# Optimization experiments

Hardware: AMD Instinct MI355X
Metric: run time of the kernel (lower is better)

The kernel has to match this reference:

```python
import jax, jax.numpy as jnp
import numpy as np

N_U = 100000; N_I = 100000; D = 64; Q = 5
N_E = 2000000; L = 2; B = 4096; P = 10
TEMP = 0.2; LAM1 = 0.2; LAM2 = 0.2
DROPOUT = 0.1; EPS = 0.1


def setup_inputs() -> dict:
    key = jax.random.key(0)
    ks = jax.random.split(key, 20)
    s = 0.05  # xavier-ish init scale
    return {
        'E_u_0': jax.random.normal(ks[0], (N_U, D), jnp.float32) * s,
        'E_i_0': jax.random.normal(ks[1], (N_I, D), jnp.float32) * s,
        'adj_vals': jax.random.uniform(ks[2], (N_E,), jnp.float32) * 0.05,
        'u_mul_s': jax.random.normal(ks[3], (N_U, Q), jnp.float32) * s,
        'v_mul_s': jax.random.normal(ks[4], (N_I, Q), jnp.float32) * s,
        'ut': jax.random.normal(ks[5], (Q, N_U), jnp.float32) * s,
        'vt': jax.random.normal(ks[6], (Q, N_I), jnp.float32) * s,
        'W_nn': jax.random.normal(ks[7], (D, D), jnp.float32) * s,
        'W_dd': jax.random.normal(ks[8], (D, D), jnp.float32) * s,
        'W_ng': jax.random.normal(ks[9], (L, D, D), jnp.float32) * s,
        'W_dg': jax.random.normal(ks[10], (L, D, D), jnp.float32) * s,
        'W_nd': jax.random.normal(ks[11], (L, D, D), jnp.float32) * s,
        'adj_rows': jax.random.randint(ks[12], (N_E,), 0, N_U),
        'adj_cols': jax.random.randint(ks[13], (N_E,), 0, N_I),
        'uids': jax.random.randint(ks[14], (B,), 0, N_U),
        'iids': jax.random.randint(ks[15], (B,), 0, N_I),
        'pos': jax.random.randint(ks[16], (B, P), 0, N_I),
        'neg': jax.random.randint(ks[17], (B, P), 0, N_I),
    }


def _act(x):  # LeakyReLU(0.5)
    return jnp.where(x >= 0, x, 0.5 * x)


def _l2n(x):  # F.normalize(p=2, dim=1)
    return x / jnp.maximum(jnp.linalg.norm(x, axis=1, keepdims=True), 1e-12)


def _spmm(vals, rows, cols, X, n_out):
    # out[r] = sum_e vals[e] * X[cols[e]]
    return jax.ops.segment_sum(vals[:, None] * X[cols], rows, num_segments=n_out)


def _info_nce(gnn_raw, hyper_raw, W, mask):
    gnn = _l2n(gnn_raw)
    hyper = _l2n(hyper_raw) @ W
    pos_score = jnp.exp(jnp.sum(gnn * hyper, axis=1) / TEMP)
    neg_score = jnp.exp(gnn @ hyper.T / TEMP).sum(axis=1)
    return (-jnp.log(pos_score / (neg_score + 1e-8) + 1e-8) * mask).sum()


def _mk_mask(k):
    return (jax.random.uniform(k, (B,)) > 0.5).astype(jnp.float32)


def _forward(E_u_0, E_i_0, adj_vals, u_mul_s, v_mul_s, ut, vt, W_nn, W_dd, W_ng, W_dg, W_nd,
             adj_rows, adj_cols, uids, iids, pos, neg):
    rkey = jax.random.key(42)
    keep = 1.0 - DROPOUT
    E_u_list = [E_u_0]; E_i_list = [E_i_0]
    Z_u_list = [None]; Z_i_list = [None]
    Z_du_list = [None]; Z_di_list = [None]
    G_u_list = [None]; G_i_list = [None]
    for _ in range(L):
        rkey, k1, k2, k3, k4 = jax.random.split(rkey, 5)
        Eu_p, Ei_p = E_u_list[-1], E_i_list[-1]
        # sparse dropout (independent masks, as in torch code) + spmm + LeakyReLU
        v1 = adj_vals * jax.random.bernoulli(k1, keep, adj_vals.shape) / keep
        Z_du = _act(_spmm(v1, adj_rows, adj_cols, Ei_p, N_U))
        v2 = adj_vals * jax.random.bernoulli(k2, keep, adj_vals.shape) / keep
        Z_di = _act(_spmm(v2, adj_cols, adj_rows, Eu_p, N_I))
        # noise-augmented view
        Z_u = _act(_spmm(adj_vals, adj_rows, adj_cols, Ei_p, N_U))
        Z_u = Z_u + jnp.sign(Z_u) * _l2n(jax.random.uniform(k3, Eu_p.shape)) * EPS
        Z_i = _act(_spmm(adj_vals, adj_cols, adj_rows, Eu_p, N_I))
        Z_i = Z_i + jnp.sign(Z_i) * _l2n(jax.random.uniform(k4, Ei_p.shape)) * EPS
        # SVD (global) view
        G_u = _act(u_mul_s @ (vt @ Ei_p))
        G_i = _act(v_mul_s @ (ut @ Eu_p))
        Z_u_list.append(Z_u); Z_i_list.append(Z_i)
        Z_du_list.append(Z_du); Z_di_list.append(Z_di)
        G_u_list.append(G_u); G_i_list.append(G_i)
        E_u_list.append(Z_u + Z_du + Eu_p)
        E_i_list.append(Z_i + Z_di + Ei_p)
    E_u = E_u_list[0]
    for t in E_u_list[1:]:
        E_u = E_u + t
    E_i = E_i_list[0]
    for t in E_i_list[1:]:
        E_i = E_i + t

    mkey = jax.random.key(7)
    def L_loss(ids, Zl, Gl, Wstack, key):
        out = jnp.float32(0.0)
        for l in range(1, L + 1):
            key, km = jax.random.split(key)
            out = out + _info_nce(Zl[l][ids], Gl[l][ids], Wstack[l - 1], _mk_mask(km))
        return out, key
    def inter_loss(ids, Zl, W, key):
        key, km = jax.random.split(key)
        return _info_nce(Zl[1][ids], Zl[2][ids], W, _mk_mask(km)), key

    loss_n_u, mkey = L_loss(uids, Z_u_list, G_u_list, W_ng, mkey)
    loss_n_i, mkey = L_loss(iids, Z_i_list, G_i_list, W_ng, mkey)
    loss_nn_u, mkey = inter_loss(uids, Z_u_list, W_nn, mkey)
    loss_nn_i, mkey = inter_loss(iids, Z_i_list, W_nn, mkey)
    loss_d_u, mkey = L_loss(uids, Z_du_list, G_u_list, W_dg, mkey)
    loss_d_i, mkey = L_loss(iids, Z_di_list, G_i_list, W_dg, mkey)
    loss_dd_u, mkey = inter_loss(uids, Z_du_list, W_dd, mkey)
    loss_dd_i, mkey = inter_loss(iids, Z_di_list, W_dd, mkey)
    loss_nd_u, mkey = L_loss(uids, Z_u_list, Z_du_list, W_nd, mkey)
    loss_nd_i, mkey = L_loss(iids, Z_i_list, Z_di_list, W_nd, mkey)
    loss_n = loss_n_u + loss_n_i
    loss_d = loss_d_u + loss_d_i
    loss_nn = loss_nn_u + loss_nn_i
    loss_dd = loss_dd_u + loss_dd_i
    loss_nd = loss_nd_u + loss_nd_i

    # U_IConstLoss, vectorized over the batch
    u_emb = E_u[uids]                       # [B, D]
    pos_emb = E_i[pos]                      # [B, P, D]
    neg_emb = E_i[neg]                      # [B, P, D]
    pos_sc = jnp.einsum('bd,bpd->bp', u_emb, pos_emb)
    neg_sc = jnp.einsum('bd,bpd->bp', u_emb, neg_emb)
    pos_d = pos_sc.min(axis=1)
    neg_d = neg_sc.max(axis=1)
    hard = jnp.where(neg_d - pos_d > 0.005, 10.0 * (neg_d - pos_d), 0.0)
    bpr = jnp.maximum(1.0 - pos_sc + neg_sc, 0.0).sum(axis=1)
    loss_r = (bpr + hard).sum() / B

    loss = loss_r + LAM1 * (loss_n + loss_d) + LAM2 * (loss_nn + loss_dd + loss_nd)
    return (loss, loss_r, loss_d, loss_n)


def reference(E_u_0, E_i_0, adj_vals, u_mul_s, v_mul_s, ut, vt, W_nn, W_dd, W_ng, W_dg, W_nd,
              adj_rows, adj_cols, uids, iids, pos, neg):
    return _forward(E_u_0, E_i_0, adj_vals, u_mul_s, v_mul_s, ut, vt, W_nn, W_dd, W_ng, W_dg, W_nd,
                    adj_rows, adj_cols, uids, iids, pos, neg)
```

## Files before the change

### kernel.cpp

```cpp
#include <hip/hip_runtime.h>
#include <hip/hip_bf16.h>
#include <cstdint>

#define C_NU 100000
#define C_NI 100000
#define C_DIM 64
#define C_Q 5
#define C_NE 2000000
#define C_B 4096
#define C_P 10
#define NROW 100000
#define NCB 196
#define NCHK 256
#define CHUNK 7813

typedef unsigned short u16;
typedef unsigned char u8;
typedef __attribute__((ext_vector_type(8))) short short8;
typedef __attribute__((ext_vector_type(4))) float f32x4;

__device__ static inline int rfl(int v) { return __builtin_amdgcn_readfirstlane(v); }
__device__ static inline uint32_t rflu(uint32_t v) {
  return (uint32_t)__builtin_amdgcn_readfirstlane((int)v);
}

__host__ __device__ static inline void tf2x32(uint32_t k0, uint32_t k1,
                                              uint32_t& x0, uint32_t& x1) {
  uint32_t k2 = k0 ^ k1 ^ 0x1BD11BDAu;
#define TFR(r) { x0 += x1; x1 = (x1 << r) | (x1 >> (32 - r)); x1 ^= x0; }
  x0 += k0; x1 += k1;
  TFR(13) TFR(15) TFR(26) TFR(6)
  x0 += k1; x1 += k2 + 1u;
  TFR(17) TFR(29) TFR(16) TFR(24)
  x0 += k2; x1 += k0 + 2u;
  TFR(13) TFR(15) TFR(26) TFR(6)
  x0 += k0; x1 += k1 + 3u;
  TFR(17) TFR(29) TFR(16) TFR(24)
  x0 += k1; x1 += k2 + 4u;
  TFR(13) TFR(15) TFR(26) TFR(6)
  x0 += k2; x1 += k0 + 5u;
#undef TFR
}

__device__ static inline float tf_uniform(uint32_t k0, uint32_t k1, uint32_t idx) {
  uint32_t x0 = 0u, x1 = idx;
  tf2x32(k0, k1, x0, x1);
  uint32_t bits = x0 ^ x1;
  return __uint_as_float((bits >> 9) | 0x3F800000u) - 1.0f;
}

__device__ static inline float leaky(float x) { return x >= 0.f ? x : 0.5f * x; }

__device__ static inline u16 f2bf(float f) {
  uint32_t x = __float_as_uint(f);
  return (u16)((x + 0x7FFFu + ((x >> 16) & 1u)) >> 16);
}
__device__ static inline float bf2f(u16 u) {
  return __uint_as_float((uint32_t)u << 16);
}

__device__ static inline u8 f2fp8(float x) {
  float t = x * 256.f;
  uint32_t sgn = (__float_as_uint(t) >> 24) & 0x80u;
  float a = fabsf(t) * 0x1p-120f;
  uint32_t u = __float_as_uint(a);
  u += 0x7FFFFu + ((u >> 20) & 1u);
  uint32_t mag = u >> 20;
  if (mag > 0x7Fu) mag = 0x7Fu;
  return (u8)(sgn | mag);
}

__constant__ int c_gsel[16] = {0,1,2,3, 0,2, 4,5,6,7, 4,6, 0,1,2,3};
__constant__ int c_hsrc[16] = {8,9,10,11, 1,3, 8,9,10,11, 5,7, 4,5,6,7};
__constant__ int c_wsel[16] = {0,1,0,1, 2,2, 3,4,3,4, 5,5, 6,7,6,7};
__constant__ int c_slot[16] = {0,0,0,0, 2,2, 1,1,1,1, 3,3, 4,4,4,4};

struct WPtrs { const float* W[8]; };
struct NceKeys { uint32_t k0[16]; uint32_t k1[16]; };
struct DropKeys { uint32_t a[8]; };


__global__ __launch_bounds__(256) void passA_hist(
    const int* __restrict__ rows, const int* __restrict__ cols,
    uint32_t* __restrict__ cntA) {
  __shared__ uint32_t h[NCB];
  const int dir = blockIdx.y, c = blockIdx.x, t = threadIdx.x;
  for (int i = t; i < NCB; i += 256) h[i] = 0u;
  __syncthreads();
  const int e0 = c * CHUNK, e1 = min(e0 + CHUNK, C_NE);
  const int* ids = dir ? cols : rows;
  for (int e = e0 + t; e < e1; e += 256) atomicAdd(&h[ids[e] >> 9], 1u);
  __syncthreads();
  for (int i = t; i < NCB; i += 256) cntA[(dir * NCB + i) * NCHK + c] = h[i];
}

__global__ __launch_bounds__(512) void scanA1(
    const uint32_t* __restrict__ cntA, uint32_t* __restrict__ offs,
    uint32_t* __restrict__ bsum) {
  __shared__ uint32_t s[512];
  const int b = blockIdx.x, t = threadIdx.x;
  const int idx = b * 512 + t;
  uint32_t v = cntA[idx];
  s[t] = v;
  __syncthreads();
  for (int off = 1; off < 512; off <<= 1) {
    uint32_t a = (t >= off) ? s[t - off] : 0u;
    __syncthreads();
    s[t] += a;
    __syncthreads();
  }
  offs[idx] = s[t] - v;
  if (t == 511) bsum[b] = s[511];
}

__global__ __launch_bounds__(256) void scanA2(
    const uint32_t* __restrict__ bsum, uint32_t* __restrict__ boff) {
  __shared__ uint32_t s[256];
  const int t = threadIdx.x;
  uint32_t v = (t < NCB) ? bsum[t] : 0u;
  s[t] = v;
  __syncthreads();
  for (int off = 1; off < 256; off <<= 1) {
    uint32_t a = (t >= off) ? s[t - off] : 0u;
    __syncthreads();
    s[t] += a;
    __syncthreads();
  }
  if (t < NCB) boff[t] = s[t] - v;
}

__global__ __launch_bounds__(512) void scanA3(
    uint32_t* __restrict__ offs, const uint32_t* __restrict__ boff) {
  offs[blockIdx.x * 512 + threadIdx.x] += boff[blockIdx.x];
}

__global__ __launch_bounds__(256) void passA_scatter(
    const int* __restrict__ rows, const int* __restrict__ cols,
    const float* __restrict__ vals, const uint32_t* __restrict__ offs,
    uint2* __restrict__ edgesA, DropKeys dk) {
  __shared__ uint32_t lofs[NCB];
  const int dir = blockIdx.y, c = blockIdx.x, t = threadIdx.x;
  for (int i = t; i < NCB; i += 256) lofs[i] = offs[(dir * NCB + i) * NCHK + c];
  __syncthreads();
  const int e0 = c * CHUNK, e1 = min(e0 + CHUNK, C_NE);
  const uint32_t kA0 = dk.a[dir * 4 + 0], kA1 = dk.a[dir * 4 + 1];
  const uint32_t kB0 = dk.a[dir * 4 + 2], kB1 = dk.a[dir * 4 + 3];
  for (int e = e0 + t; e < e1; e += 256) {
    const int r = rows[e], cc = cols[e];
    const int dst = dir ? cc : r, src = dir ? r : cc;
    const uint32_t kl0 = (tf_uniform(kA0, kA1, (uint32_t)e) < 0.9f) ? 1u : 0u;
    const uint32_t kl1 = (tf_uniform(kB0, kB1, (uint32_t)e) < 0.9f) ? 1u : 0u;
    const uint32_t x = (uint32_t)src | (kl0 << 17) | (kl1 << 18) |
                       ((uint32_t)(dst & 511) << 19);
    const uint32_t pos = atomicAdd(&lofs[dst >> 9], 1u);
    edgesA[pos] = make_uint2(x, __float_as_uint(vals[e]));
  }
}

__global__ __launch_bounds__(512) void passB_kernel(
    const uint2* __restrict__ edgesA, const uint32_t* __restrict__ offs,
    uint2* __restrict__ edgesB, uint32_t* __restrict__ starts) {
  __shared__ uint32_t cnt[512];
  __shared__ uint32_t scn[512];
  const int dir = blockIdx.y, cb = blockIdx.x, t = threadIdx.x;
  const uint32_t segStart = offs[(dir * NCB + cb) * NCHK];
  const uint32_t segEnd = (dir == 1 && cb == NCB - 1)
                              ? (uint32_t)(2 * C_NE)
                              : offs[(dir * NCB + cb + 1) * NCHK];
  cnt[t] = 0u;
  __syncthreads();
  for (uint32_t e = segStart + t; e < segEnd; e += 512)
    atomicAdd(&cnt[(edgesA[e].x >> 19) & 511u], 1u);
  __syncthreads();
  uint32_t v = cnt[t];
  scn[t] = v;
  __syncthreads();
  for (int off = 1; off < 512; off <<= 1) {
    uint32_t a = (t >= off) ? scn[t - off] : 0u;
    __syncthreads();
    scn[t] += a;
    __syncthreads();
  }
  const uint32_t rstart = segStart + scn[t] - v;
  const int grow = cb * 512 + t;
  if (grow < NROW) starts[dir * (NROW + 1) + grow] = rstart;
  if (cb == NCB - 1 && t == 0) starts[dir * (NROW + 1) + NROW] = segEnd;
  cnt[t] = rstart;
  __syncthreads();
  for (uint32_t e = segStart + t; e < segEnd; e += 512) {
    const uint2 q = edgesA[e];
    const uint32_t pos = atomicAdd(&cnt[(q.x >> 19) & 511u], 1u);
    edgesB[pos] = q;
  }
}

__global__ __launch_bounds__(256) void fp8_convert(
    const float* __restrict__ src, u8* __restrict__ dst, int n4) {
  int i = blockIdx.x * 256 + threadIdx.x;
  if (i >= n4) return;
  float4 v = ((const float4*)src)[i];
  uint32_t o = (uint32_t)f2fp8(v.x) | ((uint32_t)f2fp8(v.y) << 8) |
               ((uint32_t)f2fp8(v.z) << 16) | ((uint32_t)f2fp8(v.w) << 24);
  ((uint32_t*)dst)[i] = o;
}

__global__ __launch_bounds__(256) void w16_prep(WPtrs wp, u16* __restrict__ Wt16) {
  int i = blockIdx.x * 256 + threadIdx.x;
  if (i >= 8 * 4096) return;
  int w = i >> 12, kd = i & 4095, k = kd >> 6, d = kd & 63;
  Wt16[w * 4096 + d * 64 + k] = f2bf(wp.W[w][k * 64 + d]);
}

__global__ __launch_bounds__(256) void spmm_row(
    const uint2* __restrict__ edges, const uint32_t* __restrict__ starts,
    const u8* __restrict__ Einf, const float* __restrict__ Eprev,
    float* __restrict__ Enext, u8* __restrict__ Enf8,
    u16* __restrict__ Zout, u16* __restrict__ Zdout,
    uint32_t nk0, uint32_t nk1, int layer) {
  const int row = rfl(blockIdx.x * 4 + (threadIdx.x >> 6));
  const int lane = threadIdx.x & 63;
  if (row >= NROW) return;
  const uint32_t s0 = rflu(starts[row]);
  const uint32_t s1 = rflu(starts[row + 1]);
  const uint32_t kbit = 1u << (17 + layer);
  const float VS = 0x1p112f;
  float z = 0.f, zd = 0.f;
  uint32_t e = s0;
  for (; e + 4 <= s1; e += 4) {
    const uint32_t p0 = rflu(edges[e].x),     w0 = rflu(edges[e].y);
    const uint32_t p1 = rflu(edges[e + 1].x), w1 = rflu(edges[e + 1].y);
    const uint32_t p2 = rflu(edges[e + 2].x), w2 = rflu(edges[e + 2].y);
    const uint32_t p3 = rflu(edges[e + 3].x), w3 = rflu(edges[e + 3].y);
    const uint32_t b0 = Einf[(size_t)(p0 & 0x1FFFFu) * 64 + lane];
    const uint32_t b1 = Einf[(size_t)(p1 & 0x1FFFFu) * 64 + lane];
    const uint32_t b2 = Einf[(size_t)(p2 & 0x1FFFFu) * 64 + lane];
    const uint32_t b3 = Einf[(size_t)(p3 & 0x1FFFFu) * 64 + lane];
    const float x0 = __uint_as_float(((b0 & 0x80u) << 24) | ((b0 & 0x7Fu) << 20));
    const float x1 = __uint_as_float(((b1 & 0x80u) << 24) | ((b1 & 0x7Fu) << 20));
    const float x2 = __uint_as_float(((b2 & 0x80u) << 24) | ((b2 & 0x7Fu) << 20));
    const float x3 = __uint_as_float(((b3 & 0x80u) << 24) | ((b3 & 0x7Fu) << 20));
    const float v0 = __uint_as_float(w0) * VS, v1 = __uint_as_float(w1) * VS;
    const float v2 = __uint_as_float(w2) * VS, v3 = __uint_as_float(w3) * VS;
    const float d0 = (p0 & kbit) ? v0 : 0.f;
    const float d1 = (p1 & kbit) ? v1 : 0.f;
    const float d2 = (p2 & kbit) ? v2 : 0.f;
    const float d3 = (p3 & kbit) ? v3 : 0.f;
    z += v0 * x0; zd += d0 * x0;
    z += v1 * x1; zd += d1 * x1;
    z += v2 * x2; zd += d2 * x2;
    z += v3 * x3; zd += d3 * x3;
  }
  for (; e < s1; ++e) {
    const uint32_t p = rflu(edges[e].x), wv = rflu(edges[e].y);
    const uint32_t b = Einf[(size_t)(p & 0x1FFFFu) * 64 + lane];
    const float x = __uint_as_float(((b & 0x80u) << 24) | ((b & 0x7Fu) << 20));
    const float v = __uint_as_float(wv) * VS;
    z += v * x;
    zd += ((p & kbit) ? v : 0.f) * x;
  }
  z = leaky(z);
  zd = leaky(zd * (1.0f / 0.9f));
  const float u = tf_uniform(nk0, nk1, (uint32_t)row * 64u + (uint32_t)lane);
  float ss = u * u;
#pragma unroll
  for (int off = 1; off < 64; off <<= 1) ss += __shfl_xor(ss, off);
  const float nrm = fmaxf(sqrtf(ss), 1e-12f);
  const float sg = (z > 0.f) ? 1.f : (z < 0.f ? -1.f : 0.f);
  z += sg * (u / nrm) * 0.1f;
  const size_t j = (size_t)row * 64 + lane;
  Zout[j] = f2bf(z);
  Zdout[j] = f2bf(zd);
  if (Enext) {
    const float en = z + zd + Eprev[j];
    Enext[j] = en;
    Enf8[j] = f2fp8(en);
  }
}

__global__ __launch_bounds__(256) void svd_reduce2(
    const float* __restrict__ T0, const float* __restrict__ E0,
    const float* __restrict__ T1, const float* __restrict__ E1,
    float* __restrict__ Mu, float* __restrict__ Mi) {
  const int dir = blockIdx.y;
  const float* __restrict__ T = dir ? T1 : T0;
  const float* __restrict__ E = dir ? E1 : E0;
  float* __restrict__ M = dir ? Mi : Mu;
  const int lane = threadIdx.x & 63;
  const int wl = threadIdx.x >> 6;
  const int gw = blockIdx.x * 4 + wl;
  float a0 = 0.f, a1 = 0.f, a2 = 0.f, a3 = 0.f, a4 = 0.f;
  for (int i = gw; i < NROW; i += 4096) {
    const float x = E[(size_t)i * 64 + lane];
    a0 += T[i] * x;
    a1 += T[NROW + i] * x;
    a2 += T[2 * NROW + i] * x;
    a3 += T[3 * NROW + i] * x;
    a4 += T[4 * NROW + i] * x;
  }
  __shared__ float red[4][5][64];
  red[wl][0][lane] = a0; red[wl][1][lane] = a1; red[wl][2][lane] = a2;
  red[wl][3][lane] = a3; red[wl][4][lane] = a4;
  __syncthreads();
  for (int o = threadIdx.x; o < 320; o += 256) {
    const int q = o >> 6, d = o & 63;
    const float s = red[0][q][d] + red[1][q][d] + red[2][q][d] + red[3][q][d];
    atomicAdd(&M[o], s);
  }
}

__global__ __launch_bounds__(256) void gather_norm(
    const int* __restrict__ ids, const u16* __restrict__ Z,
    const u16* __restrict__ Zd, const float* __restrict__ mul_s,
    const float* __restrict__ M, u16* __restrict__ oZ,
    u16* __restrict__ oZd, u16* __restrict__ oG) {
  long long t = (long long)blockIdx.x * blockDim.x + threadIdx.x;
  int b = (int)(t >> 6);
  int d = (int)(t & 63);
  if (b >= C_B) return;
  int id = rfl(ids[b]);
  float v;
  u16* out;
  if (blockIdx.y == 0) { v = bf2f(Z[(size_t)id * 64 + d]); out = oZ; }
  else if (blockIdx.y == 1) { v = bf2f(Zd[(size_t)id * 64 + d]); out = oZd; }
  else {
    float s = 0.f;
#pragma unroll
    for (int q = 0; q < 5; ++q) s += mul_s[(size_t)id * 5 + q] * M[q * 64 + d];
    v = leaky(s);
    out = oG;
  }
  float ss = v * v;
#pragma unroll
  for (int off = 1; off < 64; off <<= 1) ss += __shfl_xor(ss, off);
  float nrm = fmaxf(sqrtf(ss), 1e-12f);
  out[(size_t)b * 64 + d] = f2bf(v / nrm);
}

__global__ __launch_bounds__(256) void hyper_mfma(
    const u16* __restrict__ nb, const u16* __restrict__ Wt16,
    u16* __restrict__ hy) {
  const int call = blockIdx.y;
  const int b0 = blockIdx.x * 64;
  __shared__ u16 Xs[64 * 64];
  __shared__ u16 Ws[64 * 64];
  const int tid = threadIdx.x, lane = tid & 63, wid = tid >> 6;
  const u16* X = nb + (size_t)c_hsrc[call] * C_B * 64;
  const u16* Wt = Wt16 + (size_t)c_wsel[call] * 4096;
  {
    const int r = tid >> 2, seg = tid & 3;
    const int base = r * 128 + seg * 32, sw = (r & 7) << 4;
    const uint4* sx = (const uint4*)&X[(size_t)(b0 + r) * 64 + seg * 16];
    uint4 a = sx[0], b = sx[1];
    *(uint4*)((char*)Xs + (base ^ sw)) = a;
    *(uint4*)((char*)Xs + ((base + 16) ^ sw)) = b;
    const uint4* sv = (const uint4*)&Wt[r * 64 + seg * 16];
    uint4 c = sv[0], d = sv[1];
    *(uint4*)((char*)Ws + (base ^ sw)) = c;
    *(uint4*)((char*)Ws + ((base + 16) ^ sw)) = d;
  }
  __syncthreads();
  const int am = (wid << 4) + (lane & 15);
  short8 af[2];
#pragma unroll
  for (int ks = 0; ks < 2; ++ks) {
    const int off = (am * 128 + ks * 64 + ((lane >> 4) << 4)) ^ ((am & 7) << 4);
    af[ks] = *(const short8*)((const char*)Xs + off);
  }
  const int ob = b0 + (wid << 4) + ((lane >> 4) << 2);
#pragma unroll
  for (int n = 0; n < 4; ++n) {
    const int bn = (n << 4) + (lane & 15);
    f32x4 acc = {0.f, 0.f, 0.f, 0.f};
#pragma unroll
    for (int ks = 0; ks < 2; ++ks) {
      const int off = (bn * 128 + ks * 64 + ((lane >> 4) << 4)) ^ ((bn & 7) << 4);
      short8 bf = *(const short8*)((const char*)Ws + off);
      acc = __builtin_amdgcn_mfma_f32_16x16x32_bf16(af[ks], bf, acc, 0, 0, 0);
    }
    const int d = (n << 4) + (lane & 15);
#pragma unroll
    for (int j = 0; j < 4; ++j)
      hy[(size_t)call * C_B * 64 + (size_t)(ob + j) * 64 + d] = f2bf(acc[j]);
  }
}

__global__ __launch_bounds__(256) void nce_mfma(
    const u16* __restrict__ nb, const u16* __restrict__ hy,
    float* __restrict__ slots, NceKeys nk) {
  const int call = blockIdx.y;
  const u16* G = nb + (size_t)c_gsel[call] * C_B * 64;
  const u16* H = hy + (size_t)call * C_B * 64;
  const int br = blockIdx.x * 128;
  __shared__ u16 Gs[128 * 64];
  __shared__ u16 Hs[2][64 * 64];
  const int tid = threadIdx.x, lane = tid & 63, wid = tid >> 6;
  {
    const int r2 = tid >> 1;
    const int sw2 = (r2 & 7) << 4;
#pragma unroll
    for (int p = 0; p < 2; ++p) {
      const int sg = (tid & 1) + p * 2;
      const uint4* src = (const uint4*)&G[(size_t)(br + r2) * 64 + sg * 16];
      uint4 a = src[0], b = src[1];
      const int bse = r2 * 128 + sg * 32;
      *(uint4*)((char*)Gs + (bse ^ sw2)) = a;
      *(uint4*)((char*)Gs + ((bse + 16) ^ sw2)) = b;
    }
  }
  const int r = tid >> 2, seg = tid & 3;
  const int base = r * 128 + seg * 32, sw = (r & 7) << 4;
  {
    const uint4* src = (const uint4*)&H[(size_t)r * 64 + seg * 16];
    uint4 a = src[0], b = src[1];
    *(uint4*)((char*)Hs[0] + (base ^ sw)) = a;
    *(uint4*)((char*)Hs[0] + ((base + 16) ^ sw)) = b;
  }
  float rs[2] = {0.f, 0.f}, ps[2] = {0.f, 0.f};
  short8 bfG[2][2];
  const int jt_diag = (blockIdx.x << 1) + (wid >> 1);
  const int hsd0 = (wid & 1) << 1;
  int cur = 0;
  for (int jt = 0; jt < 64; ++jt) {
    __syncthreads();
    if (jt == 0) {
#pragma unroll
      for (int s = 0; s < 2; ++s)
#pragma unroll
        for (int ks = 0; ks < 2; ++ks) {
          const int gc = (wid << 5) + (s << 4) + (lane & 15);
          const int off = (gc * 128 + ks * 64 + ((lane >> 4) << 4)) ^ ((gc & 7) << 4);
          bfG[s][ks] = *(const short8*)((const char*)Gs + off);
        }
    }
    uint4 na, nb_;
    if (jt + 1 < 64) {
      const uint4* src = (const uint4*)&H[(size_t)((jt + 1) * 64 + r) * 64 + seg * 16];
      na = src[0]; nb_ = src[1];
    }
    const bool dj = (jt == jt_diag);
    const char* Hb = (const char*)(Hs[cur]);
#pragma unroll
    for (int hs = 0; hs < 4; ++hs) {
      const int hr = (hs << 4) + (lane & 15);
      const int offA0 = (hr * 128 + ((lane >> 4) << 4)) ^ ((hr & 7) << 4);
      const int offA1 = (hr * 128 + 64 + ((lane >> 4) << 4)) ^ ((hr & 7) << 4);
      const short8 af0 = *(const short8*)(Hb + offA0);
      const short8 af1 = *(const short8*)(Hb + offA1);
      f32x4 acc0 = {0.f, 0.f, 0.f, 0.f}, acc1 = {0.f, 0.f, 0.f, 0.f};
      __builtin_amdgcn_s_setprio(1);
      acc0 = __builtin_amdgcn_mfma_f32_16x16x32_bf16(af0, bfG[0][0], acc0, 0, 0, 0);
      acc0 = __builtin_amdgcn_mfma_f32_16x16x32_bf16(af1, bfG[0][1], acc0, 0, 0, 0);
      acc1 = __builtin_amdgcn_mfma_f32_16x16x32_bf16(af0, bfG[1][0], acc1, 0, 0, 0);
      acc1 = __builtin_amdgcn_mfma_f32_16x16x32_bf16(af1, bfG[1][1], acc1, 0, 0, 0);
      __builtin_amdgcn_s_setprio(0);
      float e0[4], e1[4];
#pragma unroll
      for (int j = 0; j < 4; ++j) {
        e0[j] = exp2f(acc0[j] * 7.2134752f);
        e1[j] = exp2f(acc1[j] * 7.2134752f);
      }
      rs[0] += (e0[0] + e0[1]) + (e0[2] + e0[3]);
      rs[1] += (e1[0] + e1[1]) + (e1[2] + e1[3]);
      if (dj) {
        const int jm = (lane & 15) - ((lane >> 4) << 2);
        if (hs == hsd0) {
#pragma unroll
          for (int j = 0; j < 4; ++j)
            if (jm == j) ps[0] = e0[j];
        }
        if (hs == hsd0 + 1) {
#pragma unroll
          for (int j = 0; j < 4; ++j)
            if (jm == j) ps[1] = e1[j];
        }
      }
    }
    if (jt + 1 < 64) {
      *(uint4*)((char*)Hs[cur ^ 1] + (base ^ sw)) = na;
      *(uint4*)((char*)Hs[cur ^ 1] + ((base + 16) ^ sw)) = nb_;
    }
    cur ^= 1;
  }
#pragma unroll
  for (int s = 0; s < 2; ++s) {
    rs[s] += __shfl_xor(rs[s], 16); rs[s] += __shfl_xor(rs[s], 32);
    ps[s] += __shfl_xor(ps[s], 16); ps[s] += __shfl_xor(ps[s], 32);
  }
  float c = 0.f;
  if ((lane >> 4) == 0) {
#pragma unroll
    for (int s = 0; s < 2; ++s) {
      const float v = -__logf(ps[s] / (rs[s] + 1e-8f) + 1e-8f);
      const int gg = br + (wid << 5) + (s << 4) + (lane & 15);
      const float u = tf_uniform(nk.k0[call], nk.k1[call], (uint32_t)gg);
      c += (u > 0.5f) ? v : 0.f;
    }
  }
  c += __shfl_xor(c, 1); c += __shfl_xor(c, 2);
  c += __shfl_xor(c, 4); c += __shfl_xor(c, 8);
  if (lane == 0) atomicAdd(&slots[c_slot[call]], c);
}

__global__ __launch_bounds__(256) void loss_r_kernel(
    const float* __restrict__ E0u, const float* __restrict__ Eu1,
    const u16* __restrict__ Zu, const u16* __restrict__ Zdu,
    const float* __restrict__ E0i, const float* __restrict__ Ei1,
    const u16* __restrict__ Zi, const u16* __restrict__ Zdi,
    const int* __restrict__ uids, const int* __restrict__ pos,
    const int* __restrict__ neg, float* __restrict__ slots) {
  long long t = (long long)blockIdx.x * blockDim.x + threadIdx.x;
  int b = (int)(t >> 6);
  int d = (int)(t & 63);
  if (b >= C_B) return;
  size_t ju = (size_t)rfl(uids[b]) * 64 + d;
  float u = E0u[ju] + 2.f * Eu1[ju] + bf2f(Zu[ju]) + bf2f(Zdu[ju]);
  float bpr = 0.f, pmin = 3.4e38f, nmax = -3.4e38f;
  for (int p = 0; p < C_P; ++p) {
    size_t jp = (size_t)rfl(pos[b * C_P + p]) * 64 + d;
    size_t jn = (size_t)rfl(neg[b * C_P + p]) * 64 + d;
    float pe = E0i[jp] + 2.f * Ei1[jp] + bf2f(Zi[jp]) + bf2f(Zdi[jp]);
    float ne = E0i[jn] + 2.f * Ei1[jn] + bf2f(Zi[jn]) + bf2f(Zdi[jn]);
    float psc = u * pe, nsc = u * ne;
#pragma unroll
    for (int off = 1; off < 64; off <<= 1) {
      psc += __shfl_xor(psc, off);
      nsc += __shfl_xor(nsc, off);
    }
    pmin = fminf(pmin, psc);
    nmax = fmaxf(nmax, nsc);
    bpr += fmaxf(1.f - psc + nsc, 0.f);
  }
  if (d == 0) {
    float hd = (nmax - pmin > 0.005f) ? 10.f * (nmax - pmin) : 0.f;
    atomicAdd(&slots[5], bpr + hd);
  }
}

__global__ void final_kernel(const float* __restrict__ slots, float* __restrict__ out) {
  if (threadIdx.x == 0 && blockIdx.x == 0) {
    float n = slots[0], dl = slots[1], nn = slots[2], dd = slots[3], nd = slots[4];
    float lr = slots[5] / (float)C_B;
    out[0] = lr + 0.2f * (n + dl) + 0.2f * (nn + dd + nd);
    out[1] = lr;
    out[2] = dl;
    out[3] = n;
  }
}

extern "C" void kernel_launch(void* const* d_in, const int* in_sizes, int n_in,
                              void* d_out, int out_size, void* d_ws, size_t ws_size,
                              hipStream_t stream) {
  (void)in_sizes; (void)n_in; (void)out_size;
  const float* E_u_0   = (const float*)d_in[0];
  const float* E_i_0   = (const float*)d_in[1];
  const float* adjvals = (const float*)d_in[2];
  const float* u_mul_s = (const float*)d_in[3];
  const float* v_mul_s = (const float*)d_in[4];
  const float* ut      = (const float*)d_in[5];
  const float* vt      = (const float*)d_in[6];
  const float* W_nn    = (const float*)d_in[7];
  const float* W_dd    = (const float*)d_in[8];
  const float* W_ng    = (const float*)d_in[9];
  const float* W_dg    = (const float*)d_in[10];
  const float* W_nd    = (const float*)d_in[11];
  const int* adj_rows  = (const int*)d_in[12];
  const int* adj_cols  = (const int*)d_in[13];
  const int* uids      = (const int*)d_in[14];
  const int* iids      = (const int*)d_in[15];
  const int* pos       = (const int*)d_in[16];
  const int* neg       = (const int*)d_in[17];
  float* out = (float*)d_out;

  const size_t NU64 = (size_t)C_NU * 64;
  const size_t NI64 = (size_t)C_NI * 64;
  const size_t B64  = (size_t)C_B * 64;

  float* w = (float*)d_ws;
  float* Eu1 = w; w += NU64;
  float* Ei1 = w; w += NI64;
  u16* Zu  = (u16*)w;
  u16* Zdu = Zu + NU64;
  u16* Zi  = Zdu + NU64;
  u16* Zdi = Zi + NI64;
  w += 2 * NU64;
  float* Mu = w; w += 512;
  float* Mi = w; w += 512;
  u16* normbuf16 = (u16*)w; w += 6 * B64;
  float* slots = w; w += 16;
  uint2* edgesB = (uint2*)w; w += 4 * C_NE;
  u16* hyper16 = (u16*)edgesB;
  u16* Wt16 = (u16*)w; w += 16384;
  uint32_t* cntA = (uint32_t*)w; w += NCB * NCHK * 2;
  uint32_t* offs = (uint32_t*)w; w += NCB * NCHK * 2;
  uint32_t* bsumA = (uint32_t*)w; w += NCB;
  uint32_t* boffA = (uint32_t*)w; w += NCB;
  uint32_t* startsAbs = (uint32_t*)w; w += 2 * (NROW + 1);
  u8* Eu0f = (u8*)w; w += NU64 / 4;
  u8* Ei0f = (u8*)w; w += NI64 / 4;
  u8* Eu1f = (u8*)w; w += NU64 / 4;
  u8* Ei1f = Ei0f;
  uint2* edgesA = (uint2*)Zu;
  if ((size_t)((char*)w - (char*)d_ws) > ws_size) return;

  auto ksplit = [](uint32_t a, uint32_t b, uint32_t idx, uint32_t& o0, uint32_t& o1) {
    uint32_t x0 = 0u, x1 = idx;
    tf2x32(a, b, x0, x1);
    o0 = x0; o1 = x1;
  };
  uint32_t rk0 = 0u, rk1 = 42u;
  uint32_t lk[2][4][2];
  for (int l = 0; l < 2; ++l) {
    uint32_t n0, n1;
    ksplit(rk0, rk1, 0u, n0, n1);
    for (int i = 0; i < 4; ++i) ksplit(rk0, rk1, (uint32_t)(i + 1), lk[l][i][0], lk[l][i][1]);
    rk0 = n0; rk1 = n1;
  }
  NceKeys nk;
  {
    uint32_t mk0 = 0u, mk1 = 7u;
    for (int i = 0; i < 16; ++i) {
      uint32_t n0, n1;
      ksplit(mk0, mk1, 0u, n0, n1);
      ksplit(mk0, mk1, 1u, nk.k0[i], nk.k1[i]);
      mk0 = n0; mk1 = n1;
    }
  }
  DropKeys dk;
  dk.a[0] = lk[0][0][0]; dk.a[1] = lk[0][0][1];
  dk.a[2] = lk[1][0][0]; dk.a[3] = lk[1][0][1];
  dk.a[4] = lk[0][1][0]; dk.a[5] = lk[0][1][1];
  dk.a[6] = lk[1][1][0]; dk.a[7] = lk[1][1][1];
  WPtrs wp;
  wp.W[0] = W_ng; wp.W[1] = W_ng + 4096;
  wp.W[2] = W_nn;
  wp.W[3] = W_dg; wp.W[4] = W_dg + 4096;
  wp.W[5] = W_dd;
  wp.W[6] = W_nd; wp.W[7] = W_nd + 4096;

  hipMemsetAsync(slots, 0, 16 * 4, stream);
  passA_hist<<<dim3(NCHK, 2), 256, 0, stream>>>(adj_rows, adj_cols, cntA);
  scanA1<<<NCB, 512, 0, stream>>>(cntA, offs, bsumA);
  scanA2<<<1, 256, 0, stream>>>(bsumA, boffA);
  scanA3<<<NCB, 512, 0, stream>>>(offs, boffA);
  passA_scatter<<<dim3(NCHK, 2), 256, 0, stream>>>(
      adj_rows, adj_cols, adjvals, offs, edgesA, dk);
  passB_kernel<<<dim3(NCB, 2), 512, 0, stream>>>(edgesA, offs, edgesB, startsAbs);
  fp8_convert<<<(int)(NU64 / 4 + 255) / 256, 256, 0, stream>>>(E_u_0, Eu0f, (int)(NU64 / 4));
  fp8_convert<<<(int)(NI64 / 4 + 255) / 256, 256, 0, stream>>>(E_i_0, Ei0f, (int)(NI64 / 4));
  w16_prep<<<(8 * 4096 + 255) / 256, 256, 0, stream>>>(wp, Wt16);

  const int gb = (int)(B64 / 256);
  const int sb = (NROW + 3) / 4;

  for (int l = 0; l < 2; ++l) {
    hipMemsetAsync(Mu, 0, 1024 * 4, stream);
    svd_reduce2<<<dim3(1024, 2), 256, 0, stream>>>(
        vt, (l == 0) ? E_i_0 : Ei1, ut, (l == 0) ? E_u_0 : Eu1, Mu, Mi);
    spmm_row<<<sb, 256, 0, stream>>>(
        edgesB, startsAbs, (l == 0) ? Ei0f : Ei1f,
        (l == 0) ? E_u_0 : nullptr, (l == 0) ? Eu1 : nullptr,
        (l == 0) ? Eu1f : nullptr, Zu, Zdu, lk[l][2][0], lk[l][2][1], l);
    spmm_row<<<sb, 256, 0, stream>>>(
        edgesB, startsAbs + (NROW + 1), (l == 0) ? Eu0f : Eu1f,
        (l == 0) ? E_i_0 : nullptr, (l == 0) ? Ei1 : nullptr,
        (l == 0) ? Ei1f : nullptr, Zi, Zdi, lk[l][3][0], lk[l][3][1], l);
    gather_norm<<<dim3(gb, 3), 256, 0, stream>>>(
        uids, Zu, Zdu, u_mul_s, Mu,
        normbuf16 + (size_t)(0 + l) * B64, normbuf16 + (size_t)(4 + l) * B64,
        normbuf16 + (size_t)(8 + l) * B64);
    gather_norm<<<dim3(gb, 3), 256, 0, stream>>>(
        iids, Zi, Zdi, v_mul_s, Mi,
        normbuf16 + (size_t)(2 + l) * B64, normbuf16 + (size_t)(6 + l) * B64,
        normbuf16 + (size_t)(10 + l) * B64);
  }

  hyper_mfma<<<dim3(C_B / 64, 16), 256, 0, stream>>>(normbuf16, Wt16, hyper16);
  nce_mfma<<<dim3(C_B / 128, 16), 256, 0, stream>>>(normbuf16, hyper16, slots, nk);
  loss_r_kernel<<<gb, 256, 0, stream>>>(E_u_0, Eu1, Zu, Zdu, E_i_0, Ei1, Zi, Zdi,
                                        uids, pos, neg, slots);
  final_kernel<<<1, 1, 0, stream>>>(slots, out);
}
```

Measured before the change: 687.1 us.

## Split NCE column loop across blocks with partial row-sum buffers and final pass

```diff
diff --git a/kernel.cpp b/kernel.cpp
--- a/kernel.cpp
+++ b/kernel.cpp
@@ -380,17 +380,20 @@
     const int d = (n << 4) + (lane & 15);
 #pragma unroll
     for (int j = 0; j < 4; ++j)
-      hy[(size_t)call * C_B * 64 + (size_t)(ob + j) * 64 + d] = f2bf(acc[j]);
-  }
-}
-
-__global__ __launch_bounds__(256) void nce_mfma(
+      hy[(size_t)call * C_B * 64 + (size_t)(ob + j) * 64 + d] =
+          f2bf(acc[j] * 7.2134752f);
+  }
+}
+
+__global__ __launch_bounds__(256) void nce_partial(
     const u16* __restrict__ nb, const u16* __restrict__ hy,
-    float* __restrict__ slots, NceKeys nk) {
-  const int call = blockIdx.y;
+    float* __restrict__ rsbuf, float* __restrict__ psbuf) {
+  const int call = blockIdx.z;
+  const int jc = blockIdx.y;
   const u16* G = nb + (size_t)c_gsel[call] * C_B * 64;
   const u16* H = hy + (size_t)call * C_B * 64;
   const int br = blockIdx.x * 128;
+  const int jt0 = jc * 16;
   __shared__ u16 Gs[128 * 64];
   __shared__ u16 Hs[2][64 * 64];
   const int tid = threadIdx.x, lane = tid & 63, wid = tid >> 6;
@@ -410,7 +413,7 @@
   const int r = tid >> 2, seg = tid & 3;
   const int base = r * 128 + seg * 32, sw = (r & 7) << 4;
   {
-    const uint4* src = (const uint4*)&H[(size_t)r * 64 + seg * 16];
+    const uint4* src = (const uint4*)&H[(size_t)(jt0 * 64 + r) * 64 + seg * 16];
     uint4 a = src[0], b = src[1];
     *(uint4*)((char*)Hs[0] + (base ^ sw)) = a;
     *(uint4*)((char*)Hs[0] + ((base + 16) ^ sw)) = b;
@@ -420,9 +423,9 @@
   const int jt_diag = (blockIdx.x << 1) + (wid >> 1);
   const int hsd0 = (wid & 1) << 1;
   int cur = 0;
-  for (int jt = 0; jt < 64; ++jt) {
+  for (int jt = jt0; jt < jt0 + 16; ++jt) {
     __syncthreads();
-    if (jt == 0) {
+    if (jt == jt0) {
 #pragma unroll
       for (int s = 0; s < 2; ++s)
 #pragma unroll
@@ -433,7 +436,7 @@
         }
     }
     uint4 na, nb_;
-    if (jt + 1 < 64) {
+    if (jt + 1 < jt0 + 16) {
       const uint4* src = (const uint4*)&H[(size_t)((jt + 1) * 64 + r) * 64 + seg * 16];
       na = src[0]; nb_ = src[1];
     }
@@ -456,8 +459,8 @@
       float e0[4], e1[4];
 #pragma unroll
       for (int j = 0; j < 4; ++j) {
-        e0[j] = exp2f(acc0[j] * 7.2134752f);
-        e1[j] = exp2f(acc1[j] * 7.2134752f);
+        e0[j] = exp2f(acc0[j]);
+        e1[j] = exp2f(acc1[j]);
       }
       rs[0] += (e0[0] + e0[1]) + (e0[2] + e0[3]);
       rs[1] += (e1[0] + e1[1]) + (e1[2] + e1[3]);
@@ -475,7 +478,7 @@
         }
       }
     }
-    if (jt + 1 < 64) {
+    if (jt + 1 < jt0 + 16) {
       *(uint4*)((char*)Hs[cur ^ 1] + (base ^ sw)) = na;
       *(uint4*)((char*)Hs[cur ^ 1] + ((base + 16) ^ sw)) = nb_;
     }
@@ -486,19 +489,34 @@
     rs[s] += __shfl_xor(rs[s], 16); rs[s] += __shfl_xor(rs[s], 32);
     ps[s] += __shfl_xor(ps[s], 16); ps[s] += __shfl_xor(ps[s], 32);
   }
-  float c = 0.f;
   if ((lane >> 4) == 0) {
+    const bool own_diag = ((jt_diag >> 4) == jc);
 #pragma unroll
     for (int s = 0; s < 2; ++s) {
-      const float v = -__logf(ps[s] / (rs[s] + 1e-8f) + 1e-8f);
       const int gg = br + (wid << 5) + (s << 4) + (lane & 15);
-      const float u = tf_uniform(nk.k0[call], nk.k1[call], (uint32_t)gg);
-      c += (u > 0.5f) ? v : 0.f;
-    }
-  }
-  c += __shfl_xor(c, 1); c += __shfl_xor(c, 2);
-  c += __shfl_xor(c, 4); c += __shfl_xor(c, 8);
-  if (lane == 0) atomicAdd(&slots[c_slot[call]], c);
+      atomicAdd(&rsbuf[(size_t)call * C_B + gg], rs[s]);
+      if (own_diag) psbuf[(size_t)call * C_B + gg] = ps[s];
+    }
+  }
+}
+
+__global__ __launch_bounds__(256) void nce_final(
+    const float* __restrict__ rsbuf, const float* __restrict__ psbuf,
+    float* __restrict__ slots, NceKeys nk) {
+  const int call = blockIdx.y;
+  const int g = blockIdx.x * 256 + threadIdx.x;
+  const float rs = rsbuf[(size_t)call * C_B + g];
+  const float ps = psbuf[(size_t)call * C_B + g];
+  const float v = -__logf(ps / (rs + 1e-8f) + 1e-8f);
+  const float u = tf_uniform(nk.k0[call], nk.k1[call], (uint32_t)g);
+  float c = (u > 0.5f) ? v : 0.f;
+#pragma unroll
+  for (int off = 1; off < 64; off <<= 1) c += __shfl_xor(c, off);
+  __shared__ float wsum[4];
+  if ((threadIdx.x & 63) == 0) wsum[threadIdx.x >> 6] = c;
+  __syncthreads();
+  if (threadIdx.x == 0)
+    atomicAdd(&slots[c_slot[call]], wsum[0] + wsum[1] + wsum[2] + wsum[3]);
 }
 
 __global__ __launch_bounds__(256) void loss_r_kernel(
@@ -599,6 +617,8 @@
   u8* Ei0f = (u8*)w; w += NI64 / 4;
   u8* Eu1f = (u8*)w; w += NU64 / 4;
   u8* Ei1f = Ei0f;
+  float* rsbuf = w; w += 16 * C_B;
+  float* psbuf = w; w += 16 * C_B;
   uint2* edgesA = (uint2*)Zu;
   if ((size_t)((char*)w - (char*)d_ws) > ws_size) return;
 
@@ -638,6 +658,7 @@
   wp.W[6] = W_nd; wp.W[7] = W_nd + 4096;
 
   hipMemsetAsync(slots, 0, 16 * 4, stream);
+  hipMemsetAsync(rsbuf, 0, 16 * C_B * 4, stream);
   passA_hist<<<dim3(NCHK, 2), 256, 0, stream>>>(adj_rows, adj_cols, cntA);
   scanA1<<<NCB, 512, 0, stream>>>(cntA, offs, bsumA);
   scanA2<<<1, 256, 0, stream>>>(bsumA, boffA);
@@ -675,7 +696,9 @@
   }
 
   hyper_mfma<<<dim3(C_B / 64, 16), 256, 0, stream>>>(normbuf16, Wt16, hyper16);
-  nce_mfma<<<dim3(C_B / 128, 16), 256, 0, stream>>>(normbuf16, hyper16, slots, nk);
+  nce_partial<<<dim3(C_B / 128, 4, 16), 256, 0, stream>>>(normbuf16, hyper16,
+                                                          rsbuf, psbuf);
+  nce_final<<<dim3(C_B / 256, 16), 256, 0, stream>>>(rsbuf, psbuf, slots, nk);
   loss_r_kernel<<<gb, 256, 0, stream>>>(E_u_0, Eu1, Zu, Zdu, E_i_0, Ei1, Zi, Zdi,
                                         uids, pos, neg, slots);
   final_kernel<<<1, 1, 0, stream>>>(slots, out);
```

Result: faster. 655.2 us (-4.6%).
